# Kernel tuning notes

Measured on AMD Instinct MI355X. Metric: run time of the kernel, lower is better.

Reference implementation:

```python
import jax, jax.numpy as jnp
import numpy as np

N_NODES = 50000
N_EDGES = 600000
NUM_GRAPHS = 64


def gcn_conv(x, W, b, src, dst, n):
    # PyG GCNConv: x' = D^{-1/2} (A + I) D^{-1/2} (x W) + b, self-loops implicit
    h = x @ W  # [N, H]
    deg = jax.ops.segment_sum(jnp.ones((src.shape[0],), h.dtype), dst, num_segments=n) + 1.0
    dinv = jax.lax.rsqrt(deg)  # [N]
    norm = dinv[src] * dinv[dst]  # [E]
    msg = h[src] * norm[:, None]  # [E, H] gather + scale
    agg = jax.ops.segment_sum(msg, dst, num_segments=n)  # scatter-add
    agg = agg + h * (dinv * dinv)[:, None]  # self-loop contribution
    return agg + b


def global_mean_pool(x, batch, num_graphs):
    s = jax.ops.segment_sum(x, batch, num_segments=num_graphs)
    cnt = jax.ops.segment_sum(jnp.ones((x.shape[0],), x.dtype), batch, num_segments=num_graphs)
    return s / jnp.maximum(cnt, 1.0)[:, None]


def setup_inputs() -> dict:
    key = jax.random.key(0)
    ks = jax.random.split(key, 12)
    x = jax.random.normal(ks[0], (N_NODES, 128), jnp.float32)
    edge_index = jax.random.randint(ks[1], (2, N_EDGES), 0, N_NODES, jnp.int64)
    batch = jnp.sort(jax.random.randint(ks[2], (N_NODES,), 0, NUM_GRAPHS, jnp.int64))
    W1 = jax.random.normal(ks[3], (128, 128), jnp.float32) * 0.08
    b1 = jax.random.normal(ks[4], (128,), jnp.float32) * 0.02
    W2 = jax.random.normal(ks[5], (128, 128), jnp.float32) * 0.08
    b2 = jax.random.normal(ks[6], (128,), jnp.float32) * 0.02
    Wfc1 = jax.random.normal(ks[7], (128, 64), jnp.float32) * 0.08
    bfc1 = jax.random.normal(ks[8], (64,), jnp.float32) * 0.02
    Wfc2 = jax.random.normal(ks[9], (64, 1), jnp.float32) * 0.08
    bfc2 = jax.random.normal(ks[10], (1,), jnp.float32) * 0.02
    return {"x": x, "edge_index": edge_index, "batch": batch,
            "W1": W1, "b1": b1, "W2": W2, "b2": b2,
            "Wfc1": Wfc1, "bfc1": bfc1, "Wfc2": Wfc2, "bfc2": bfc2}


def reference(x, edge_index, batch, W1, b1, W2, b2, Wfc1, bfc1, Wfc2, bfc2):
    n = x.shape[0]
    src, dst = edge_index[0], edge_index[1]
    h = jax.nn.relu(gcn_conv(x, W1, b1, src, dst, n))
    # dropout = identity (eval mode)
    h = jax.nn.relu(gcn_conv(h, W2, b2, src, dst, n))
    g = global_mean_pool(h, batch, NUM_GRAPHS)  # [G, H]
    g = jax.nn.relu(g @ Wfc1 + bfc1)
    return g @ Wfc2 + bfc2  # [G, 1]
```

## Files before the change

kernel.cpp:

```cpp
#include <hip/hip_runtime.h>
#include <hip/hip_fp16.h>


typedef short bf16x8 __attribute__((ext_vector_type(8)));
typedef float f32x4  __attribute__((ext_vector_type(4)));

__device__ inline unsigned short f2bf_rne(float f) {
    unsigned u = __float_as_uint(f);
    unsigned r = (u + 0x7fffu + ((u >> 16) & 1u)) >> 16;
    return (unsigned short)r;
}
__device__ inline float bf2f(unsigned short h) {
    return __uint_as_float(((unsigned)h) << 16);
}

__global__ __launch_bounds__(256) void wconv_zero(const float* __restrict__ W1,
                                                  const float* __restrict__ W2,
                                                  unsigned short* __restrict__ W1h,
                                                  unsigned short* __restrict__ W1l,
                                                  unsigned short* __restrict__ W2h,
                                                  unsigned short* __restrict__ W2l,
                                                  int* __restrict__ count,
                                                  float* __restrict__ pooled,
                                                  float* __restrict__ cnt, int N) {
    int tid = threadIdx.x;
    int b = blockIdx.x;
    if (b < 128) {
        int i = b * 256 + tid;
        const float* W = (i < 16384) ? W1 : W2;
        unsigned short* Wh = (i < 16384) ? W1h : W2h;
        unsigned short* Wl = (i < 16384) ? W1l : W2l;
        int ii = i & 16383;
        int k = ii >> 7, n = ii & 127;
        float v = W[ii];
        unsigned short h = f2bf_rne(v);
        float lo = v - bf2f(h);
        int ct = n >> 4, nn = n & 15, ks = k >> 5, q = (k >> 3) & 3, j = k & 7;
        int oidx = (((ct * 4 + ks) * 64) + (q * 16 + nn)) * 8 + j;
        Wh[oidx] = h;
        Wl[oidx] = f2bf_rne(lo);
    } else {
        int idx = (b - 128) * 256 + tid;
        if (idx < N) count[idx] = 0;
        else if (idx < N + 8192) pooled[idx - N] = 0.f;
        else if (idx < N + 8256) cnt[idx - N - 8192] = 0.f;
    }
}

__global__ __launch_bounds__(256) void scan1_kernel(const int* __restrict__ count,
                                                    int* __restrict__ tmp,
                                                    int* __restrict__ bsum, int N) {
    __shared__ int s[256];
    int tid = threadIdx.x;
    int i = blockIdx.x * 256 + tid;
    int v = (i < N) ? count[i] : 0;
    s[tid] = v;
    __syncthreads();
#pragma unroll
    for (int off = 1; off < 256; off <<= 1) {
        int t = (tid >= off) ? s[tid - off] : 0;
        __syncthreads();
        s[tid] += t;
        __syncthreads();
    }
    if (i < N) tmp[i] = s[tid];
    if (tid == 255) bsum[blockIdx.x] = s[255];
}

__global__ __launch_bounds__(256) void scan2_kernel(const int* __restrict__ bsum,
                                                    int* __restrict__ boff, int nb) {
    __shared__ int s[256];
    int tid = threadIdx.x;
    int v = (tid < nb) ? bsum[tid] : 0;
    s[tid] = v;
    __syncthreads();
#pragma unroll
    for (int off = 1; off < 256; off <<= 1) {
        int t = (tid >= off) ? s[tid - off] : 0;
        __syncthreads();
        s[tid] += t;
        __syncthreads();
    }
    if (tid < nb) boff[tid] = s[tid] - v;
}

__global__ void finalize_kernel(const int* __restrict__ count, const int* __restrict__ tmp,
                                const int* __restrict__ boff, int* __restrict__ rowptr,
                                float* __restrict__ dinv, int N) {
    int i = blockIdx.x * blockDim.x + threadIdx.x;
    if (i > N) return;
    int ex = (i == 0) ? 0 : tmp[i - 1] + boff[(i - 1) >> 8];
    rowptr[i] = ex;
    if (i < N) dinv[i] = 1.0f / sqrtf((float)count[i] + 1.0f);
}

__global__ void reorder_kernel(const int* __restrict__ src, const int* __restrict__ dst,
                               const int* __restrict__ rank,
                               const float* __restrict__ dinv,
                               const int* __restrict__ rowptr,
                               int2* __restrict__ em, int E) {
    int e = blockIdx.x * blockDim.x + threadIdx.x;
    if (e < E) {
        int s = src[e], d = dst[e];
        int pos = rowptr[d] + rank[e];
        float norm = dinv[s] * dinv[d];
        em[pos] = make_int2(s, __float_as_int(norm));
    }
}

template <bool RELU_IN>
__device__ __forceinline__ void gemm_body(const float* __restrict__ X,
                                          const unsigned short* __restrict__ Wfh,
                                          const unsigned short* __restrict__ Wfl,
                                          __half* __restrict__ OUT, int M, int blk) {
    __shared__ unsigned short Xh[64][136];
    __shared__ unsigned short Xl[64][136];
    int tid = threadIdx.x;
    int w = tid >> 6, l = tid & 63;
    int m0 = blk * 64;

#pragma unroll
    for (int it = 0; it < 8; it++) {
        int i = tid + it * 256;
        int row = i >> 5, c4 = i & 31;
        int grow = m0 + row;
        float4 v = make_float4(0.f, 0.f, 0.f, 0.f);
        if (grow < M) v = *(const float4*)(X + (size_t)grow * 128 + c4 * 4);
        if (RELU_IN) {
            v.x = fmaxf(v.x, 0.f); v.y = fmaxf(v.y, 0.f);
            v.z = fmaxf(v.z, 0.f); v.w = fmaxf(v.w, 0.f);
        }
        float a[4] = {v.x, v.y, v.z, v.w};
        ushort4 hi, lo;
        unsigned short* hp = (unsigned short*)&hi;
        unsigned short* lp = (unsigned short*)&lo;
#pragma unroll
        for (int e = 0; e < 4; e++) {
            unsigned short h = f2bf_rne(a[e]);
            hp[e] = h;
            lp[e] = f2bf_rne(a[e] - bf2f(h));
        }
        *(ushort4*)&Xh[row][c4 * 4] = hi;
        *(ushort4*)&Xl[row][c4 * 4] = lo;
    }
    __syncthreads();

    int q = l >> 4, nn = l & 15;
    f32x4 acc[8];
#pragma unroll
    for (int ct = 0; ct < 8; ct++) acc[ct] = (f32x4){0.f, 0.f, 0.f, 0.f};

#pragma unroll
    for (int ks = 0; ks < 4; ks++) {
        bf16x8 ahi = *(const bf16x8*)&Xh[w * 16 + nn][ks * 32 + q * 8];
        bf16x8 alo = *(const bf16x8*)&Xl[w * 16 + nn][ks * 32 + q * 8];
#pragma unroll
        for (int ct = 0; ct < 8; ct++) {
            size_t fo = ((size_t)(ct * 4 + ks) * 64 + l) * 8;
            bf16x8 bhi = *(const bf16x8*)(Wfh + fo);
            bf16x8 blo = *(const bf16x8*)(Wfl + fo);
            acc[ct] = __builtin_amdgcn_mfma_f32_16x16x32_bf16(ahi, bhi, acc[ct], 0, 0, 0);
            acc[ct] = __builtin_amdgcn_mfma_f32_16x16x32_bf16(alo, bhi, acc[ct], 0, 0, 0);
            acc[ct] = __builtin_amdgcn_mfma_f32_16x16x32_bf16(ahi, blo, acc[ct], 0, 0, 0);
        }
    }
    __syncthreads();

#pragma unroll
    for (int r = 0; r < 4; r++) {
        int lrow = w * 16 + q * 4 + r;
#pragma unroll
        for (int ct = 0; ct < 8; ct++) {
            __half hv = __float2half(acc[ct][r]);
            Xh[lrow][ct * 16 + nn] = __half_as_ushort(hv);
        }
    }
    __syncthreads();
#pragma unroll
    for (int t = 0; t < 4; t++) {
        int c = tid + t * 256;
        int row = c >> 4, seg = c & 15;
        int grow = m0 + row;
        if (grow < M) {
            uint4 v = *(uint4*)&Xh[row][seg * 8];
            *(uint4*)((unsigned short*)OUT + (size_t)grow * 128 + seg * 8) = v;
        }
    }
}

__global__ __launch_bounds__(256) void gemm_mfma_relu(const float* __restrict__ X,
                                                      const unsigned short* __restrict__ Wfh,
                                                      const unsigned short* __restrict__ Wfl,
                                                      __half* __restrict__ OUT, int M) {
    gemm_body<true>(X, Wfh, Wfl, OUT, M, blockIdx.x);
}

__global__ __launch_bounds__(256) void fused_hg(const float* __restrict__ X,
                                                const unsigned short* __restrict__ Wfh,
                                                const unsigned short* __restrict__ Wfl,
                                                __half* __restrict__ OUT, int M, int gblocks,
                                                const int* __restrict__ dst,
                                                int* __restrict__ count,
                                                int* __restrict__ rank, int E) {
    if ((int)blockIdx.x < gblocks) {
        gemm_body<false>(X, Wfh, Wfl, OUT, M, blockIdx.x);
    } else {
        int e = ((int)blockIdx.x - gblocks) * 256 + (int)threadIdx.x;
        if (e < E) {
            int d = dst[e];
            rank[e] = atomicAdd(&count[d], 1);
        }
    }
}

__global__ __launch_bounds__(256) void gather_half(const __half* __restrict__ h,
                                                   const float* __restrict__ dinv,
                                                   const float* __restrict__ bias,
                                                   const int* __restrict__ rowptr,
                                                   const long long* __restrict__ em,
                                                   float* __restrict__ B, int N) {
    int n = blockIdx.x * 4 + (threadIdx.x >> 6);
    int lane = threadIdx.x & 63;
    if (n >= N) return;
    int beg = rowptr[n], end = rowptr[n + 1];
    float din = dinv[n];
    const __half2* hp = (const __half2*)h;
    float2 hv = __half22float2(hp[(size_t)n * 64 + lane]);
    float sw = din * din;
    float ax = hv.x * sw, ay = hv.y * sw;
    int j = beg;
    for (; j + 8 <= end; j += 8) {
        long long v0 = em[j],     v1 = em[j + 1], v2 = em[j + 2], v3 = em[j + 3];
        long long v4 = em[j + 4], v5 = em[j + 5], v6 = em[j + 6], v7 = em[j + 7];
        float2 r0 = __half22float2(hp[(size_t)(int)v0 * 64 + lane]);
        float2 r1 = __half22float2(hp[(size_t)(int)v1 * 64 + lane]);
        float2 r2 = __half22float2(hp[(size_t)(int)v2 * 64 + lane]);
        float2 r3 = __half22float2(hp[(size_t)(int)v3 * 64 + lane]);
        float2 r4 = __half22float2(hp[(size_t)(int)v4 * 64 + lane]);
        float2 r5 = __half22float2(hp[(size_t)(int)v5 * 64 + lane]);
        float2 r6 = __half22float2(hp[(size_t)(int)v6 * 64 + lane]);
        float2 r7 = __half22float2(hp[(size_t)(int)v7 * 64 + lane]);
        float n0 = __int_as_float((int)(v0 >> 32));
        float n1 = __int_as_float((int)(v1 >> 32));
        float n2 = __int_as_float((int)(v2 >> 32));
        float n3 = __int_as_float((int)(v3 >> 32));
        float n4 = __int_as_float((int)(v4 >> 32));
        float n5 = __int_as_float((int)(v5 >> 32));
        float n6 = __int_as_float((int)(v6 >> 32));
        float n7 = __int_as_float((int)(v7 >> 32));
        ax = fmaf(r0.x, n0, ax); ay = fmaf(r0.y, n0, ay);
        ax = fmaf(r1.x, n1, ax); ay = fmaf(r1.y, n1, ay);
        ax = fmaf(r2.x, n2, ax); ay = fmaf(r2.y, n2, ay);
        ax = fmaf(r3.x, n3, ax); ay = fmaf(r3.y, n3, ay);
        ax = fmaf(r4.x, n4, ax); ay = fmaf(r4.y, n4, ay);
        ax = fmaf(r5.x, n5, ax); ay = fmaf(r5.y, n5, ay);
        ax = fmaf(r6.x, n6, ax); ay = fmaf(r6.y, n6, ay);
        ax = fmaf(r7.x, n7, ax); ay = fmaf(r7.y, n7, ay);
    }
    for (; j + 4 <= end; j += 4) {
        long long v0 = em[j], v1 = em[j + 1], v2 = em[j + 2], v3 = em[j + 3];
        float2 r0 = __half22float2(hp[(size_t)(int)v0 * 64 + lane]);
        float2 r1 = __half22float2(hp[(size_t)(int)v1 * 64 + lane]);
        float2 r2 = __half22float2(hp[(size_t)(int)v2 * 64 + lane]);
        float2 r3 = __half22float2(hp[(size_t)(int)v3 * 64 + lane]);
        float n0 = __int_as_float((int)(v0 >> 32));
        float n1 = __int_as_float((int)(v1 >> 32));
        float n2 = __int_as_float((int)(v2 >> 32));
        float n3 = __int_as_float((int)(v3 >> 32));
        ax = fmaf(r0.x, n0, ax); ay = fmaf(r0.y, n0, ay);
        ax = fmaf(r1.x, n1, ax); ay = fmaf(r1.y, n1, ay);
        ax = fmaf(r2.x, n2, ax); ay = fmaf(r2.y, n2, ay);
        ax = fmaf(r3.x, n3, ax); ay = fmaf(r3.y, n3, ay);
    }
    for (; j < end; j++) {
        long long v = em[j];
        float2 r = __half22float2(hp[(size_t)(int)v * 64 + lane]);
        float nr = __int_as_float((int)(v >> 32));
        ax = fmaf(r.x, nr, ax); ay = fmaf(r.y, nr, ay);
    }
    float2 o;
    o.x = ax + bias[lane * 2];
    o.y = ay + bias[lane * 2 + 1];
    *(float2*)(B + (size_t)n * 128 + lane * 2) = o;
}

__global__ __launch_bounds__(256) void pool_kernel(const float* __restrict__ B,
                                                   const int* __restrict__ batch,
                                                   float* pooled, float* cnt, int N) {
    int c = threadIdx.x & 127;
    int half = threadIdx.x >> 7;
    int n0 = blockIdx.x * 128;
    float acc = 0.f, cacc = 0.f;
    int curg = -1;
    for (int i = half; i < 128; i += 2) {
        int n = n0 + i;
        if (n >= N) break;
        int g = batch[n];
        float v = fmaxf(B[(size_t)n * 128 + c], 0.f);
        if (g != curg) {
            if (curg >= 0) {
                atomicAdd(&pooled[curg * 128 + c], acc);
                if (c == 0) atomicAdd(&cnt[curg], cacc);
            }
            curg = g; acc = 0.f; cacc = 0.f;
        }
        acc += v; cacc += 1.f;
    }
    if (curg >= 0) {
        atomicAdd(&pooled[curg * 128 + c], acc);
        if (c == 0) atomicAdd(&cnt[curg], cacc);
    }
}

__global__ __launch_bounds__(64) void head_kernel(const float* __restrict__ pooled,
                                                  const float* __restrict__ cnt,
                                                  const float* __restrict__ Wfc1,
                                                  const float* __restrict__ bfc1,
                                                  const float* __restrict__ Wfc2,
                                                  const float* __restrict__ bfc2,
                                                  float* __restrict__ out) {
    __shared__ float mean[128];
    int g = blockIdx.x;
    int t = threadIdx.x;
    float inv = 1.0f / fmaxf(cnt[g], 1.0f);
    mean[t] = pooled[g * 128 + t] * inv;
    mean[t + 64] = pooled[g * 128 + t + 64] * inv;
    __syncthreads();
    float s = bfc1[t];
#pragma unroll 4
    for (int k = 0; k < 128; k++) s = fmaf(mean[k], Wfc1[k * 64 + t], s);
    float p = fmaxf(s, 0.f) * Wfc2[t];
#pragma unroll
    for (int o = 32; o > 0; o >>= 1) p += __shfl_down(p, o, 64);
    if (t == 0) out[g] = p + bfc2[0];
}

extern "C" void kernel_launch(void* const* d_in, const int* in_sizes, int n_in,
                              void* d_out, int out_size, void* d_ws, size_t ws_size,
                              hipStream_t stream) {
    const float* x    = (const float*)d_in[0];
    const int*   edge = (const int*)d_in[1];
    const int*   batch= (const int*)d_in[2];
    const float* W1   = (const float*)d_in[3];
    const float* b1   = (const float*)d_in[4];
    const float* W2   = (const float*)d_in[5];
    const float* b2   = (const float*)d_in[6];
    const float* Wfc1 = (const float*)d_in[7];
    const float* bfc1 = (const float*)d_in[8];
    const float* Wfc2 = (const float*)d_in[9];
    const float* bfc2 = (const float*)d_in[10];
    float* out = (float*)d_out;

    int N = in_sizes[0] / 128;
    int E = in_sizes[1] / 2;
    const int* src = edge;
    const int* dst = edge + E;

    char* ws = (char*)d_ws;
    size_t off = 0;
    auto alloc = [&](size_t bytes) { void* p = ws + off; off += (bytes + 255) & ~(size_t)255; return p; };
    __half* Ah    = (__half*)alloc((size_t)N * 128 * sizeof(__half));
    float* B      = (float*)alloc((size_t)N * 128 * sizeof(float));
    float* dinv   = (float*)alloc((size_t)N * sizeof(float));
    int*   count  = (int*)alloc((size_t)N * sizeof(int));
    int*   tmp    = (int*)alloc((size_t)N * sizeof(int));
    int*   rowptr = (int*)alloc((size_t)(N + 1) * sizeof(int));
    int*   rank   = (int*)alloc((size_t)E * sizeof(int));
    int2*  em     = (int2*)alloc((size_t)E * sizeof(int2));
    int*   bsum   = (int*)alloc(256 * sizeof(int));
    int*   boff   = (int*)alloc(256 * sizeof(int));
    float* pooled = (float*)alloc(64 * 128 * sizeof(float));
    float* cnt    = (float*)alloc(64 * sizeof(float));
    unsigned short* W1h = (unsigned short*)alloc(16384 * sizeof(short));
    unsigned short* W1l = (unsigned short*)alloc(16384 * sizeof(short));
    unsigned short* W2h = (unsigned short*)alloc(16384 * sizeof(short));
    unsigned short* W2l = (unsigned short*)alloc(16384 * sizeof(short));

    int nb = (N + 255) / 256;
    int hb = (E + 255) / 256;
    int gblocks = (N + 63) / 64;
    int ablocks = (N + 3) / 4;
    int zb = (N + 8256 + 255) / 256;

    wconv_zero<<<128 + zb, 256, 0, stream>>>(W1, W2, W1h, W1l, W2h, W2l,
                                             count, pooled, cnt, N);

    fused_hg<<<gblocks + hb, 256, 0, stream>>>(x, W1h, W1l, Ah, N, gblocks,
                                               dst, count, rank, E);

    scan1_kernel<<<nb, 256, 0, stream>>>(count, tmp, bsum, N);
    scan2_kernel<<<1, 256, 0, stream>>>(bsum, boff, nb);
    finalize_kernel<<<(N + 256) / 256, 256, 0, stream>>>(count, tmp, boff, rowptr, dinv, N);
    reorder_kernel<<<hb, 256, 0, stream>>>(src, dst, rank, dinv, rowptr, em, E);

    gather_half<<<ablocks, 256, 0, stream>>>(Ah, dinv, b1, rowptr, (const long long*)em, B, N);

    gemm_mfma_relu<<<gblocks, 256, 0, stream>>>(B, W2h, W2l, Ah, N);
    gather_half<<<ablocks, 256, 0, stream>>>(Ah, dinv, b2, rowptr, (const long long*)em, B, N);

    pool_kernel<<<(N + 127) / 128, 256, 0, stream>>>(B, batch, pooled, cnt, N);
    head_kernel<<<64, 64, 0, stream>>>(pooled, cnt, Wfc1, bfc1, Wfc2, bfc2, out);
}
```

Baseline: 247.2 us.

## Fuse CSR build and pool/head kernels with grid barriers; prefetch edge metadata

Merges the scan, block-offset, finalize and reorder kernels into one persistent kernel that uses a software grid barrier. Pool and head are merged the same way, which cuts kernel launch count and the gaps between launches. The gather loop now software-pipelines the next batch of eight edge entries while the current one is accumulated. The grid barriers rely on all blocks being co-resident (196 and 391 blocks), which risks deadlock if they are not, and each barrier adds spin-wait cost.

```diff
diff --git a/kernel.cpp b/kernel.cpp
--- a/kernel.cpp
+++ b/kernel.cpp
@@ -12,6 +12,24 @@
 }
 __device__ inline float bf2f(unsigned short h) {
     return __uint_as_float(((unsigned)h) << 16);
+}
+
+__device__ inline void gbar(int* cnt, int* gen, int nblk) {
+    __threadfence();
+    __syncthreads();
+    if (threadIdx.x == 0) {
+        int g = __hip_atomic_load(gen, __ATOMIC_RELAXED, __HIP_MEMORY_SCOPE_AGENT);
+        if (__hip_atomic_fetch_add(cnt, 1, __ATOMIC_ACQ_REL, __HIP_MEMORY_SCOPE_AGENT) == nblk - 1) {
+            __hip_atomic_store(cnt, 0, __ATOMIC_RELAXED, __HIP_MEMORY_SCOPE_AGENT);
+            __hip_atomic_store(gen, g + 1, __ATOMIC_RELEASE, __HIP_MEMORY_SCOPE_AGENT);
+        } else {
+            while (__hip_atomic_load(gen, __ATOMIC_ACQUIRE, __HIP_MEMORY_SCOPE_AGENT) == g) {
+                __builtin_amdgcn_s_sleep(1);
+            }
+        }
+    }
+    __syncthreads();
+    __threadfence();
 }
 
 __global__ __launch_bounds__(256) void wconv_zero(const float* __restrict__ W1,
@@ -22,7 +40,8 @@
                                                   unsigned short* __restrict__ W2l,
                                                   int* __restrict__ count,
                                                   float* __restrict__ pooled,
-                                                  float* __restrict__ cnt, int N) {
+                                                  float* __restrict__ cnt,
+                                                  int* __restrict__ sync, int N) {
     int tid = threadIdx.x;
     int b = blockIdx.x;
     if (b < 128) {
@@ -44,67 +63,7 @@
         if (idx < N) count[idx] = 0;
         else if (idx < N + 8192) pooled[idx - N] = 0.f;
         else if (idx < N + 8256) cnt[idx - N - 8192] = 0.f;
-    }
-}
-
-__global__ __launch_bounds__(256) void scan1_kernel(const int* __restrict__ count,
-                                                    int* __restrict__ tmp,
-                                                    int* __restrict__ bsum, int N) {
-    __shared__ int s[256];
-    int tid = threadIdx.x;
-    int i = blockIdx.x * 256 + tid;
-    int v = (i < N) ? count[i] : 0;
-    s[tid] = v;
-    __syncthreads();
-#pragma unroll
-    for (int off = 1; off < 256; off <<= 1) {
-        int t = (tid >= off) ? s[tid - off] : 0;
-        __syncthreads();
-        s[tid] += t;
-        __syncthreads();
-    }
-    if (i < N) tmp[i] = s[tid];
-    if (tid == 255) bsum[blockIdx.x] = s[255];
-}
-
-__global__ __launch_bounds__(256) void scan2_kernel(const int* __restrict__ bsum,
-                                                    int* __restrict__ boff, int nb) {
-    __shared__ int s[256];
-    int tid = threadIdx.x;
-    int v = (tid < nb) ? bsum[tid] : 0;
-    s[tid] = v;
-    __syncthreads();
-#pragma unroll
-    for (int off = 1; off < 256; off <<= 1) {
-        int t = (tid >= off) ? s[tid - off] : 0;
-        __syncthreads();
-        s[tid] += t;
-        __syncthreads();
-    }
-    if (tid < nb) boff[tid] = s[tid] - v;
-}
-
-__global__ void finalize_kernel(const int* __restrict__ count, const int* __restrict__ tmp,
-                                const int* __restrict__ boff, int* __restrict__ rowptr,
-                                float* __restrict__ dinv, int N) {
-    int i = blockIdx.x * blockDim.x + threadIdx.x;
-    if (i > N) return;
-    int ex = (i == 0) ? 0 : tmp[i - 1] + boff[(i - 1) >> 8];
-    rowptr[i] = ex;
-    if (i < N) dinv[i] = 1.0f / sqrtf((float)count[i] + 1.0f);
-}
-
-__global__ void reorder_kernel(const int* __restrict__ src, const int* __restrict__ dst,
-                               const int* __restrict__ rank,
-                               const float* __restrict__ dinv,
-                               const int* __restrict__ rowptr,
-                               int2* __restrict__ em, int E) {
-    int e = blockIdx.x * blockDim.x + threadIdx.x;
-    if (e < E) {
-        int s = src[e], d = dst[e];
-        int pos = rowptr[d] + rank[e];
-        float norm = dinv[s] * dinv[d];
-        em[pos] = make_int2(s, __float_as_int(norm));
+        else if (idx < N + 8260) sync[idx - N - 8256] = 0;
     }
 }
 
@@ -212,6 +171,98 @@
         }
     }
 }
+
+__global__ __launch_bounds__(256) void fused_csr(const int* __restrict__ count,
+                                                 int* __restrict__ tmp,
+                                                 int* __restrict__ bsum,
+                                                 int* __restrict__ boff,
+                                                 int* __restrict__ rowptr,
+                                                 float* __restrict__ dinv,
+                                                 const int* __restrict__ src,
+                                                 const int* __restrict__ dst,
+                                                 const int* __restrict__ rank,
+                                                 int2* __restrict__ em,
+                                                 int* __restrict__ sync,
+                                                 int N, int E, int nb) {
+    int tid = threadIdx.x;
+    int b = blockIdx.x;
+    __shared__ int s[256];
+
+    {
+        int i = b * 256 + tid;
+        int v = (i < N) ? count[i] : 0;
+        s[tid] = v;
+        __syncthreads();
+#pragma unroll
+        for (int off = 1; off < 256; off <<= 1) {
+            int t = (tid >= off) ? s[tid - off] : 0;
+            __syncthreads();
+            s[tid] += t;
+            __syncthreads();
+        }
+        if (i < N) tmp[i] = s[tid];
+        if (tid == 255) bsum[b] = s[255];
+    }
+    gbar(&sync[0], &sync[1], nb);
+
+    if (b == 0) {
+        int v = (tid < nb) ? bsum[tid] : 0;
+        s[tid] = v;
+        __syncthreads();
+#pragma unroll
+        for (int off = 1; off < 256; off <<= 1) {
+            int t = (tid >= off) ? s[tid - off] : 0;
+            __syncthreads();
+            s[tid] += t;
+            __syncthreads();
+        }
+        if (tid < nb) boff[tid] = s[tid] - v;
+    }
+    gbar(&sync[0], &sync[1], nb);
+
+    for (int i = b * 256 + tid; i <= N; i += nb * 256) {
+        int ex = (i == 0) ? 0 : tmp[i - 1] + boff[(i - 1) >> 8];
+        rowptr[i] = ex;
+        if (i < N) dinv[i] = 1.0f / sqrtf((float)count[i] + 1.0f);
+    }
+    for (int e = b * 256 + tid; e < E; e += nb * 256) {
+        int sv = src[e], d = dst[e];
+        int ex = (d == 0) ? 0 : tmp[d - 1] + boff[(d - 1) >> 8];
+        int pos = ex + rank[e];
+        float ds = 1.0f / sqrtf((float)count[sv] + 1.0f);
+        float dd = 1.0f / sqrtf((float)count[d] + 1.0f);
+        float norm = ds * dd;
+        em[pos] = make_int2(sv, __float_as_int(norm));
+    }
+}
+
+#define BATCH8(va0, va1, va2, va3, va4, va5, va6, va7)                          \
+    do {                                                                        \
+        float2 r0 = __half22float2(hp[(size_t)(int)(va0) * 64 + lane]);         \
+        float2 r1 = __half22float2(hp[(size_t)(int)(va1) * 64 + lane]);         \
+        float2 r2 = __half22float2(hp[(size_t)(int)(va2) * 64 + lane]);         \
+        float2 r3 = __half22float2(hp[(size_t)(int)(va3) * 64 + lane]);         \
+        float2 r4 = __half22float2(hp[(size_t)(int)(va4) * 64 + lane]);         \
+        float2 r5 = __half22float2(hp[(size_t)(int)(va5) * 64 + lane]);         \
+        float2 r6 = __half22float2(hp[(size_t)(int)(va6) * 64 + lane]);         \
+        float2 r7 = __half22float2(hp[(size_t)(int)(va7) * 64 + lane]);         \
+        float n0 = __int_as_float((int)((va0) >> 32));                          \
+        float n1 = __int_as_float((int)((va1) >> 32));                          \
+        float n2 = __int_as_float((int)((va2) >> 32));                          \
+        float n3 = __int_as_float((int)((va3) >> 32));                          \
+        float n4 = __int_as_float((int)((va4) >> 32));                          \
+        float n5 = __int_as_float((int)((va5) >> 32));                          \
+        float n6 = __int_as_float((int)((va6) >> 32));                          \
+        float n7 = __int_as_float((int)((va7) >> 32));                          \
+        ax = fmaf(r0.x, n0, ax); ay = fmaf(r0.y, n0, ay);                       \
+        ax = fmaf(r1.x, n1, ax); ay = fmaf(r1.y, n1, ay);                       \
+        ax = fmaf(r2.x, n2, ax); ay = fmaf(r2.y, n2, ay);                       \
+        ax = fmaf(r3.x, n3, ax); ay = fmaf(r3.y, n3, ay);                       \
+        ax = fmaf(r4.x, n4, ax); ay = fmaf(r4.y, n4, ay);                       \
+        ax = fmaf(r5.x, n5, ax); ay = fmaf(r5.y, n5, ay);                       \
+        ax = fmaf(r6.x, n6, ax); ay = fmaf(r6.y, n6, ay);                       \
+        ax = fmaf(r7.x, n7, ax); ay = fmaf(r7.y, n7, ay);                       \
+    } while (0)
 
 __global__ __launch_bounds__(256) void gather_half(const __half* __restrict__ h,
                                                    const float* __restrict__ dinv,
@@ -229,33 +280,18 @@
     float sw = din * din;
     float ax = hv.x * sw, ay = hv.y * sw;
     int j = beg;
-    for (; j + 8 <= end; j += 8) {
+    if (j + 8 <= end) {
         long long v0 = em[j],     v1 = em[j + 1], v2 = em[j + 2], v3 = em[j + 3];
         long long v4 = em[j + 4], v5 = em[j + 5], v6 = em[j + 6], v7 = em[j + 7];
-        float2 r0 = __half22float2(hp[(size_t)(int)v0 * 64 + lane]);
-        float2 r1 = __half22float2(hp[(size_t)(int)v1 * 64 + lane]);
-        float2 r2 = __half22float2(hp[(size_t)(int)v2 * 64 + lane]);
-        float2 r3 = __half22float2(hp[(size_t)(int)v3 * 64 + lane]);
-        float2 r4 = __half22float2(hp[(size_t)(int)v4 * 64 + lane]);
-        float2 r5 = __half22float2(hp[(size_t)(int)v5 * 64 + lane]);
-        float2 r6 = __half22float2(hp[(size_t)(int)v6 * 64 + lane]);
-        float2 r7 = __half22float2(hp[(size_t)(int)v7 * 64 + lane]);
-        float n0 = __int_as_float((int)(v0 >> 32));
-        float n1 = __int_as_float((int)(v1 >> 32));
-        float n2 = __int_as_float((int)(v2 >> 32));
-        float n3 = __int_as_float((int)(v3 >> 32));
-        float n4 = __int_as_float((int)(v4 >> 32));
-        float n5 = __int_as_float((int)(v5 >> 32));
-        float n6 = __int_as_float((int)(v6 >> 32));
-        float n7 = __int_as_float((int)(v7 >> 32));
-        ax = fmaf(r0.x, n0, ax); ay = fmaf(r0.y, n0, ay);
-        ax = fmaf(r1.x, n1, ax); ay = fmaf(r1.y, n1, ay);
-        ax = fmaf(r2.x, n2, ax); ay = fmaf(r2.y, n2, ay);
-        ax = fmaf(r3.x, n3, ax); ay = fmaf(r3.y, n3, ay);
-        ax = fmaf(r4.x, n4, ax); ay = fmaf(r4.y, n4, ay);
-        ax = fmaf(r5.x, n5, ax); ay = fmaf(r5.y, n5, ay);
-        ax = fmaf(r6.x, n6, ax); ay = fmaf(r6.y, n6, ay);
-        ax = fmaf(r7.x, n7, ax); ay = fmaf(r7.y, n7, ay);
+        for (; j + 16 <= end; j += 8) {
+            long long w0 = em[j + 8],  w1 = em[j + 9],  w2 = em[j + 10], w3 = em[j + 11];
+            long long w4 = em[j + 12], w5 = em[j + 13], w6 = em[j + 14], w7 = em[j + 15];
+            BATCH8(v0, v1, v2, v3, v4, v5, v6, v7);
+            v0 = w0; v1 = w1; v2 = w2; v3 = w3;
+            v4 = w4; v5 = w5; v6 = w6; v7 = w7;
+        }
+        BATCH8(v0, v1, v2, v3, v4, v5, v6, v7);
+        j += 8;
     }
     for (; j + 4 <= end; j += 4) {
         long long v0 = em[j], v1 = em[j + 1], v2 = em[j + 2], v3 = em[j + 3];
@@ -284,9 +320,16 @@
     *(float2*)(B + (size_t)n * 128 + lane * 2) = o;
 }
 
-__global__ __launch_bounds__(256) void pool_kernel(const float* __restrict__ B,
-                                                   const int* __restrict__ batch,
-                                                   float* pooled, float* cnt, int N) {
+__global__ __launch_bounds__(256) void pool_head(const float* __restrict__ B,
+                                                 const int* __restrict__ batch,
+                                                 float* pooled, float* cnt,
+                                                 const float* __restrict__ Wfc1,
+                                                 const float* __restrict__ bfc1,
+                                                 const float* __restrict__ Wfc2,
+                                                 const float* __restrict__ bfc2,
+                                                 float* __restrict__ out,
+                                                 int* __restrict__ sync,
+                                                 int N, int nblk) {
     int c = threadIdx.x & 127;
     int half = threadIdx.x >> 7;
     int n0 = blockIdx.x * 128;
@@ -310,29 +353,26 @@
         atomicAdd(&pooled[curg * 128 + c], acc);
         if (c == 0) atomicAdd(&cnt[curg], cacc);
     }
-}
-
-__global__ __launch_bounds__(64) void head_kernel(const float* __restrict__ pooled,
-                                                  const float* __restrict__ cnt,
-                                                  const float* __restrict__ Wfc1,
-                                                  const float* __restrict__ bfc1,
-                                                  const float* __restrict__ Wfc2,
-                                                  const float* __restrict__ bfc2,
-                                                  float* __restrict__ out) {
-    __shared__ float mean[128];
+
+    gbar(&sync[2], &sync[3], nblk);
+
     int g = blockIdx.x;
-    int t = threadIdx.x;
-    float inv = 1.0f / fmaxf(cnt[g], 1.0f);
-    mean[t] = pooled[g * 128 + t] * inv;
-    mean[t + 64] = pooled[g * 128 + t + 64] * inv;
-    __syncthreads();
-    float s = bfc1[t];
+    if (g < 64) {
+        __shared__ float mean[128];
+        int t = threadIdx.x;
+        float inv = 1.0f / fmaxf(cnt[g], 1.0f);
+        if (t < 128) mean[t] = pooled[g * 128 + t] * inv;
+        __syncthreads();
+        if (t < 64) {
+            float s = bfc1[t];
 #pragma unroll 4
-    for (int k = 0; k < 128; k++) s = fmaf(mean[k], Wfc1[k * 64 + t], s);
-    float p = fmaxf(s, 0.f) * Wfc2[t];
-#pragma unroll
-    for (int o = 32; o > 0; o >>= 1) p += __shfl_down(p, o, 64);
-    if (t == 0) out[g] = p + bfc2[0];
+            for (int k = 0; k < 128; k++) s = fmaf(mean[k], Wfc1[k * 64 + t], s);
+            float p = fmaxf(s, 0.f) * Wfc2[t];
+#pragma unroll
+            for (int o = 32; o > 0; o >>= 1) p += __shfl_down(p, o, 64);
+            if (t == 0) out[g] = p + bfc2[0];
+        }
+    }
 }
 
 extern "C" void kernel_launch(void* const* d_in, const int* in_sizes, int n_in,
@@ -371,6 +411,7 @@
     int*   boff   = (int*)alloc(256 * sizeof(int));
     float* pooled = (float*)alloc(64 * 128 * sizeof(float));
     float* cnt    = (float*)alloc(64 * sizeof(float));
+    int*   syncv  = (int*)alloc(4 * sizeof(int));
     unsigned short* W1h = (unsigned short*)alloc(16384 * sizeof(short));
     unsigned short* W1l = (unsigned short*)alloc(16384 * sizeof(short));
     unsigned short* W2h = (unsigned short*)alloc(16384 * sizeof(short));
@@ -380,24 +421,24 @@
     int hb = (E + 255) / 256;
     int gblocks = (N + 63) / 64;
     int ablocks = (N + 3) / 4;
-    int zb = (N + 8256 + 255) / 256;
+    int pb = (N + 127) / 128;
+    int zb = (N + 8192 + 64 + 4 + 255) / 256;
 
     wconv_zero<<<128 + zb, 256, 0, stream>>>(W1, W2, W1h, W1l, W2h, W2l,
-                                             count, pooled, cnt, N);
+                                             count, pooled, cnt, syncv, N);
 
     fused_hg<<<gblocks + hb, 256, 0, stream>>>(x, W1h, W1l, Ah, N, gblocks,
                                                dst, count, rank, E);
 
-    scan1_kernel<<<nb, 256, 0, stream>>>(count, tmp, bsum, N);
-    scan2_kernel<<<1, 256, 0, stream>>>(bsum, boff, nb);
-    finalize_kernel<<<(N + 256) / 256, 256, 0, stream>>>(count, tmp, boff, rowptr, dinv, N);
-    reorder_kernel<<<hb, 256, 0, stream>>>(src, dst, rank, dinv, rowptr, em, E);
+    fused_csr<<<nb, 256, 0, stream>>>(count, tmp, bsum, boff, rowptr, dinv,
+                                      src, dst, rank, em, syncv, N, E, nb);
 
     gather_half<<<ablocks, 256, 0, stream>>>(Ah, dinv, b1, rowptr, (const long long*)em, B, N);
 
     gemm_mfma_relu<<<gblocks, 256, 0, stream>>>(B, W2h, W2l, Ah, N);
+
     gather_half<<<ablocks, 256, 0, stream>>>(Ah, dinv, b2, rowptr, (const long long*)em, B, N);
 
-    pool_kernel<<<(N + 127) / 128, 256, 0, stream>>>(B, batch, pooled, cnt, N);
-    head_kernel<<<64, 64, 0, stream>>>(pooled, cnt, Wfc1, bfc1, Wfc2, bfc2, out);
-}
+    pool_head<<<pb, 256, 0, stream>>>(B, batch, pooled, cnt,
+                                      Wfc1, bfc1, Wfc2, bfc2, out, syncv, N, pb);
+}
```

Result: slower. 420.0 us (+69.9%).

## Split each node's edge list across four 16-lane subgroups with 16-byte gathers

Applied to the files above, without the earlier changes.

The half-precision neighbor gather now splits each wavefront into four 16-lane subgroups. Each subgroup handles a different edge and loads a full 256-byte row using 16-byte vector loads. Partial sums are combined with cross-subgroup shuffles, and one subgroup writes the float4 results. The aim is more memory-level parallelism and wider loads per edge. The cost is extra shuffle reductions, plus wasted masked lanes when a node has fewer than 16 edges (average degree is about 12).

```diff
diff --git a/kernel.cpp b/kernel.cpp
--- a/kernel.cpp
+++ b/kernel.cpp
@@ -222,66 +222,98 @@
     int n = blockIdx.x * 4 + (threadIdx.x >> 6);
     int lane = threadIdx.x & 63;
     if (n >= N) return;
+    int sub = lane >> 4, cl = lane & 15;
     int beg = rowptr[n], end = rowptr[n + 1];
-    float din = dinv[n];
-    const __half2* hp = (const __half2*)h;
-    float2 hv = __half22float2(hp[(size_t)n * 64 + lane]);
-    float sw = din * din;
-    float ax = hv.x * sw, ay = hv.y * sw;
-    int j = beg;
-    for (; j + 8 <= end; j += 8) {
-        long long v0 = em[j],     v1 = em[j + 1], v2 = em[j + 2], v3 = em[j + 3];
-        long long v4 = em[j + 4], v5 = em[j + 5], v6 = em[j + 6], v7 = em[j + 7];
-        float2 r0 = __half22float2(hp[(size_t)(int)v0 * 64 + lane]);
-        float2 r1 = __half22float2(hp[(size_t)(int)v1 * 64 + lane]);
-        float2 r2 = __half22float2(hp[(size_t)(int)v2 * 64 + lane]);
-        float2 r3 = __half22float2(hp[(size_t)(int)v3 * 64 + lane]);
-        float2 r4 = __half22float2(hp[(size_t)(int)v4 * 64 + lane]);
-        float2 r5 = __half22float2(hp[(size_t)(int)v5 * 64 + lane]);
-        float2 r6 = __half22float2(hp[(size_t)(int)v6 * 64 + lane]);
-        float2 r7 = __half22float2(hp[(size_t)(int)v7 * 64 + lane]);
-        float n0 = __int_as_float((int)(v0 >> 32));
-        float n1 = __int_as_float((int)(v1 >> 32));
-        float n2 = __int_as_float((int)(v2 >> 32));
-        float n3 = __int_as_float((int)(v3 >> 32));
-        float n4 = __int_as_float((int)(v4 >> 32));
-        float n5 = __int_as_float((int)(v5 >> 32));
-        float n6 = __int_as_float((int)(v6 >> 32));
-        float n7 = __int_as_float((int)(v7 >> 32));
-        ax = fmaf(r0.x, n0, ax); ay = fmaf(r0.y, n0, ay);
-        ax = fmaf(r1.x, n1, ax); ay = fmaf(r1.y, n1, ay);
-        ax = fmaf(r2.x, n2, ax); ay = fmaf(r2.y, n2, ay);
-        ax = fmaf(r3.x, n3, ax); ay = fmaf(r3.y, n3, ay);
-        ax = fmaf(r4.x, n4, ax); ay = fmaf(r4.y, n4, ay);
-        ax = fmaf(r5.x, n5, ax); ay = fmaf(r5.y, n5, ay);
-        ax = fmaf(r6.x, n6, ax); ay = fmaf(r6.y, n6, ay);
-        ax = fmaf(r7.x, n7, ax); ay = fmaf(r7.y, n7, ay);
-    }
-    for (; j + 4 <= end; j += 4) {
-        long long v0 = em[j], v1 = em[j + 1], v2 = em[j + 2], v3 = em[j + 3];
-        float2 r0 = __half22float2(hp[(size_t)(int)v0 * 64 + lane]);
-        float2 r1 = __half22float2(hp[(size_t)(int)v1 * 64 + lane]);
-        float2 r2 = __half22float2(hp[(size_t)(int)v2 * 64 + lane]);
-        float2 r3 = __half22float2(hp[(size_t)(int)v3 * 64 + lane]);
-        float n0 = __int_as_float((int)(v0 >> 32));
-        float n1 = __int_as_float((int)(v1 >> 32));
-        float n2 = __int_as_float((int)(v2 >> 32));
-        float n3 = __int_as_float((int)(v3 >> 32));
-        ax = fmaf(r0.x, n0, ax); ay = fmaf(r0.y, n0, ay);
-        ax = fmaf(r1.x, n1, ax); ay = fmaf(r1.y, n1, ay);
-        ax = fmaf(r2.x, n2, ax); ay = fmaf(r2.y, n2, ay);
-        ax = fmaf(r3.x, n3, ax); ay = fmaf(r3.y, n3, ay);
-    }
-    for (; j < end; j++) {
-        long long v = em[j];
-        float2 r = __half22float2(hp[(size_t)(int)v * 64 + lane]);
-        float nr = __int_as_float((int)(v >> 32));
-        ax = fmaf(r.x, nr, ax); ay = fmaf(r.y, nr, ay);
-    }
-    float2 o;
-    o.x = ax + bias[lane * 2];
-    o.y = ay + bias[lane * 2 + 1];
-    *(float2*)(B + (size_t)n * 128 + lane * 2) = o;
+    const unsigned short* hb = (const unsigned short*)h;
+
+    float a0 = 0.f, a1 = 0.f, a2 = 0.f, a3 = 0.f;
+    float a4 = 0.f, a5 = 0.f, a6 = 0.f, a7 = 0.f;
+
+    if (sub == 0) {
+        float din = dinv[n];
+        float sw = din * din;
+        uint4 raw = *(const uint4*)(hb + (size_t)n * 128 + cl * 8);
+        const __half2* hh = (const __half2*)&raw;
+        float2 f0 = __half22float2(hh[0]);
+        float2 f1 = __half22float2(hh[1]);
+        float2 f2 = __half22float2(hh[2]);
+        float2 f3 = __half22float2(hh[3]);
+        a0 = fmaf(f0.x, sw, a0); a1 = fmaf(f0.y, sw, a1);
+        a2 = fmaf(f1.x, sw, a2); a3 = fmaf(f1.y, sw, a3);
+        a4 = fmaf(f2.x, sw, a4); a5 = fmaf(f2.y, sw, a5);
+        a6 = fmaf(f3.x, sw, a6); a7 = fmaf(f3.y, sw, a7);
+    }
+
+    for (int base = beg; base < end; base += 16) {
+        int j0 = base + sub, j1 = j0 + 4, j2 = j0 + 8, j3 = j0 + 12;
+        int e1 = end - 1;
+        long long v0 = em[min(j0, e1)];
+        long long v1 = em[min(j1, e1)];
+        long long v2 = em[min(j2, e1)];
+        long long v3 = em[min(j3, e1)];
+        float n0 = (j0 < end) ? __int_as_float((int)(v0 >> 32)) : 0.f;
+        float n1 = (j1 < end) ? __int_as_float((int)(v1 >> 32)) : 0.f;
+        float n2 = (j2 < end) ? __int_as_float((int)(v2 >> 32)) : 0.f;
+        float n3 = (j3 < end) ? __int_as_float((int)(v3 >> 32)) : 0.f;
+        uint4 r0 = *(const uint4*)(hb + (size_t)(int)v0 * 128 + cl * 8);
+        uint4 r1 = *(const uint4*)(hb + (size_t)(int)v1 * 128 + cl * 8);
+        uint4 r2 = *(const uint4*)(hb + (size_t)(int)v2 * 128 + cl * 8);
+        uint4 r3 = *(const uint4*)(hb + (size_t)(int)v3 * 128 + cl * 8);
+        {
+            const __half2* hh = (const __half2*)&r0;
+            float2 f0 = __half22float2(hh[0]), f1 = __half22float2(hh[1]);
+            float2 f2 = __half22float2(hh[2]), f3 = __half22float2(hh[3]);
+            a0 = fmaf(f0.x, n0, a0); a1 = fmaf(f0.y, n0, a1);
+            a2 = fmaf(f1.x, n0, a2); a3 = fmaf(f1.y, n0, a3);
+            a4 = fmaf(f2.x, n0, a4); a5 = fmaf(f2.y, n0, a5);
+            a6 = fmaf(f3.x, n0, a6); a7 = fmaf(f3.y, n0, a7);
+        }
+        {
+            const __half2* hh = (const __half2*)&r1;
+            float2 f0 = __half22float2(hh[0]), f1 = __half22float2(hh[1]);
+            float2 f2 = __half22float2(hh[2]), f3 = __half22float2(hh[3]);
+            a0 = fmaf(f0.x, n1, a0); a1 = fmaf(f0.y, n1, a1);
+            a2 = fmaf(f1.x, n1, a2); a3 = fmaf(f1.y, n1, a3);
+            a4 = fmaf(f2.x, n1, a4); a5 = fmaf(f2.y, n1, a5);
+            a6 = fmaf(f3.x, n1, a6); a7 = fmaf(f3.y, n1, a7);
+        }
+        {
+            const __half2* hh = (const __half2*)&r2;
+            float2 f0 = __half22float2(hh[0]), f1 = __half22float2(hh[1]);
+            float2 f2 = __half22float2(hh[2]), f3 = __half22float2(hh[3]);
+            a0 = fmaf(f0.x, n2, a0); a1 = fmaf(f0.y, n2, a1);
+            a2 = fmaf(f1.x, n2, a2); a3 = fmaf(f1.y, n2, a3);
+            a4 = fmaf(f2.x, n2, a4); a5 = fmaf(f2.y, n2, a5);
+            a6 = fmaf(f3.x, n2, a6); a7 = fmaf(f3.y, n2, a7);
+        }
+        {
+            const __half2* hh = (const __half2*)&r3;
+            float2 f0 = __half22float2(hh[0]), f1 = __half22float2(hh[1]);
+            float2 f2 = __half22float2(hh[2]), f3 = __half22float2(hh[3]);
+            a0 = fmaf(f0.x, n3, a0); a1 = fmaf(f0.y, n3, a1);
+            a2 = fmaf(f1.x, n3, a2); a3 = fmaf(f1.y, n3, a3);
+            a4 = fmaf(f2.x, n3, a4); a5 = fmaf(f2.y, n3, a5);
+            a6 = fmaf(f3.x, n3, a6); a7 = fmaf(f3.y, n3, a7);
+        }
+    }
+
+#pragma unroll
+    for (int m = 16; m < 64; m <<= 1) {
+        a0 += __shfl_xor(a0, m, 64); a1 += __shfl_xor(a1, m, 64);
+        a2 += __shfl_xor(a2, m, 64); a3 += __shfl_xor(a3, m, 64);
+        a4 += __shfl_xor(a4, m, 64); a5 += __shfl_xor(a5, m, 64);
+        a6 += __shfl_xor(a6, m, 64); a7 += __shfl_xor(a7, m, 64);
+    }
+
+    if (sub == 0) {
+        float4 o0, o1;
+        o0.x = a0 + bias[cl * 8 + 0]; o0.y = a1 + bias[cl * 8 + 1];
+        o0.z = a2 + bias[cl * 8 + 2]; o0.w = a3 + bias[cl * 8 + 3];
+        o1.x = a4 + bias[cl * 8 + 4]; o1.y = a5 + bias[cl * 8 + 5];
+        o1.z = a6 + bias[cl * 8 + 6]; o1.w = a7 + bias[cl * 8 + 7];
+        *(float4*)(B + (size_t)n * 128 + cl * 8) = o0;
+        *(float4*)(B + (size_t)n * 128 + cl * 8 + 4) = o1;
+    }
 }
 
 __global__ __launch_bounds__(256) void pool_kernel(const float* __restrict__ B,
```

After: 240.3 us. 1.03x faster.
